# Performance work log

Hardware: AMD Instinct MI355X
Metric: run time of the kernel (lower is better)

## Reference

```python
import jax, jax.numpy as jnp
import numpy as np

N, C, T, H, W = 16, 64, 30, 64, 44
PC = 64
OUT_H, OUT_W = 16, 20
T_RATE, H_RATE, W_RATE = 0.4, 4.0 / 8, 10.0 / 11  # torso
HEAD_H_RATE = 1.0 / 8
EPS = 1e-8


def setup_inputs() -> dict:
    key = jax.random.key(0)
    ks = jax.random.split(key, 8)
    x = jax.random.normal(ks[0], (N, C, T, H, W), jnp.float32)
    param_x = jax.random.normal(ks[1], (N, PC), jnp.float32)
    W1 = jax.random.normal(ks[2], (PC, PC // 2), jnp.float32) * 0.1
    b1 = jnp.zeros((PC // 2,), jnp.float32)
    W2 = jax.random.normal(ks[3], (PC // 2, 7), jnp.float32) * 0.1
    b2 = jnp.zeros((7,), jnp.float32)
    Wf = jax.random.normal(ks[4], (C, C), jnp.float32) * 0.05
    bf = jnp.zeros((C,), jnp.float32)
    return {"x": x, "param_x": param_x, "W1": W1, "b1": b1, "W2": W2, "b2": b2, "Wf": Wf, "bf": bf}


def reference(x, param_x, W1, b1, W2, b2, Wf, bf):
    n, c, t, h, w = x.shape
    dtype = x.dtype
    atten_in_t = t * T_RATE
    atten_in_h = h * H_RATE
    atten_in_w = w * W_RATE
    atten_ratio = atten_in_w / atten_in_h
    aout_h = int(round(OUT_W / atten_ratio))
    anchor_t = int(round(t / 2.0))
    anchor_x = int(round(w / 2.0))
    anchor_y = int(round(atten_in_h / 2.0 + h * HEAD_H_RATE))  # torso anchor

    # --- localization MLP (locator stand-in): param_x -> 7 params per sample ---
    hid = jnp.tanh(param_x @ W1 + b1)
    p = hid @ W2 + b2  # [N, 7]
    dt0, dx0, dy0 = p[:, 0:1], p[:, 1:2], p[:, 2:3]
    log_sigma2, log_delta_t, log_delta, log_gamma = p[:, 3:4], p[:, 4:5], p[:, 5:6], p[:, 6:7]

    dx = jnp.tanh(dx0) * atten_in_w / 2.0 + anchor_x          # [N,1]
    dy = jnp.tanh(dy0) * atten_in_h / 2.0 + anchor_y          # [N,1]
    sigma2 = jnp.exp(log_sigma2)                              # [N,1]
    delta = jnp.exp(log_delta) * W_RATE                      # [N,1]
    gamma = jax.nn.sigmoid(log_gamma)                         # [N,1]

    # --- spatial Gaussian filter banks ---
    gx = jnp.arange(OUT_W, dtype=dtype)
    gy = jnp.arange(aout_h, dtype=dtype)
    mu_x = dx + (gx - OUT_W / 2.0) * delta                    # [N, OUT_W]
    mu_y = dy + (gy - aout_h / 2.0) * delta                   # [N, aout_h]
    a = jnp.arange(w, dtype=dtype)
    b = jnp.arange(h, dtype=dtype)
    s2 = sigma2[:, :, None]                                   # [N,1,1]
    Fx = jnp.exp(-((a - mu_x[:, :, None]) ** 2) / (2.0 * s2))  # [N, OUT_W, W]
    Fy = jnp.exp(-((b - mu_y[:, :, None]) ** 2) / (2.0 * s2))  # [N, aout_h, H]
    Fx = Fx / jnp.maximum(jnp.sum(Fx, -1, keepdims=True), EPS)
    Fy = Fy / jnp.maximum(jnp.sum(Fy, -1, keepdims=True), EPS)

    # --- spatial sampling: Fy @ x @ Fx^T over the (C*T)-folded batch dim ---
    x2 = x.reshape(n, c * t, h, w)
    t1 = jnp.einsum('ndhw,nqw->ndhq', x2, Fx)                 # [N, C*T, H, OUT_W]
    g = jnp.einsum('nph,ndhq->ndpq', Fy, t1)                  # [N, C*T, aout_h, OUT_W]
    pad_t = (OUT_H - aout_h) // 2
    pad_b = OUT_H - pad_t - aout_h
    g = jnp.pad(g, ((0, 0), (0, 0), (pad_t, pad_b), (0, 0)))  # [N, C*T, OUT_H, OUT_W]

    # --- temporal linear resampling (grid_sample, align_corners=True, zero pad) ---
    dt = jnp.tanh(dt0) * atten_in_t / 2.0 + anchor_t          # [N,1]
    delta_t = jnp.exp(log_delta_t) * T_RATE                   # [N,1]
    gt = jnp.arange(t, dtype=dtype)
    mu_t = dt + (gt - t / 2.0) * delta_t                      # [N, T] raw frame positions

    gseq = g.reshape(n, c, t, OUT_H * OUT_W).transpose(0, 1, 3, 2).reshape(n, c * OUT_H * OUT_W, t)
    i0f = jnp.floor(mu_t)
    frac = mu_t - i0f
    i0 = i0f.astype(jnp.int32)
    i1 = i0 + 1

    def gather(idx):
        return jnp.take_along_axis(gseq, jnp.clip(idx, 0, t - 1)[:, None, :], axis=2)

    w0 = jnp.where((i0 >= 0) & (i0 < t), 1.0 - frac, 0.0)[:, None, :]
    w1 = jnp.where((i1 >= 0) & (i1 < t), frac, 0.0)[:, None, :]
    samp = gather(i0) * w0 + gather(i1) * w1                  # [N, C*OUT_H*OUT_W, T]
    out = samp.reshape(n, c, OUT_H, OUT_W, t).transpose(0, 1, 4, 2, 3)  # [N,C,T,OUT_H,OUT_W]

    out = out * gamma.reshape(n, 1, 1, 1, 1)
    # feature extraction: pointwise Conv3d (extractor stand-in)
    out = jnp.einsum('ncthw,oc->nothw', out, Wf) + bf[None, :, None, None, None]

    params = jnp.stack([dt[:, 0], dx[:, 0], dy[:, 0], sigma2[:, 0],
                        delta[:, 0], delta_t[:, 0], gamma[:, 0]], 0)  # [7, N]
    return out, jax.lax.stop_gradient(params)
```

## Files before the change

kernel.cpp:

```cpp
#include <hip/hip_runtime.h>
#include <math.h>

#define NN 16
#define CC 64
#define TT 30
#define HH 64
#define WW 44
#define OUTH 16
#define OUTW 20
#define HW 320

#define FX_OFF    0
#define FY_OFF    14080
#define IDX0_OFF  30464
#define IDX1_OFF  30944
#define TW0_OFF   31424
#define TW1_OFF   31904
#define GAM_OFF   32384
#define G_OFF     32400

__global__ __launch_bounds__(64) void params_kernel(
    const float* __restrict__ param_x, const float* __restrict__ W1,
    const float* __restrict__ b1, const float* __restrict__ W2,
    const float* __restrict__ b2, float* __restrict__ ws,
    float* __restrict__ params_out) {
  int n = blockIdx.x;
  int tid = threadIdx.x;
  __shared__ float px[64];
  __shared__ float hid[32];
  __shared__ float pv[7];

  px[tid] = param_x[n * 64 + tid];
  __syncthreads();
  if (tid < 32) {
    float s = b1[tid];
    #pragma unroll
    for (int k = 0; k < 64; ++k) s += px[k] * W1[k * 32 + tid];
    hid[tid] = tanhf(s);
  }
  __syncthreads();
  if (tid < 7) {
    float s = b2[tid];
    #pragma unroll
    for (int j = 0; j < 32; ++j) s += hid[j] * W2[j * 7 + tid];
    pv[tid] = s;
  }
  __syncthreads();

  float dt      = tanhf(pv[0]) * 6.0f  + 15.0f;
  float dx      = tanhf(pv[1]) * 20.0f + 22.0f;
  float dy      = tanhf(pv[2]) * 16.0f + 24.0f;
  float sigma2  = expf(pv[3]);
  float delta_t = expf(pv[4]) * 0.4f;
  float delta   = expf(pv[5]) * (10.0f / 11.0f);
  float gamma   = 1.0f / (1.0f + expf(-pv[6]));
  float inv2s2  = 1.0f / (2.0f * sigma2);

  if (tid < 20) {
    float mu = dx + ((float)tid - 10.0f) * delta;
    float vals[44];
    float s = 0.0f;
    #pragma unroll
    for (int w = 0; w < 44; ++w) {
      float d = (float)w - mu;
      float e = expf(-d * d * inv2s2);
      vals[w] = e; s += e;
    }
    float inv = 1.0f / fmaxf(s, 1e-8f);
    float* Fx = ws + FX_OFF + n * (20 * 44) + tid * 44;
    #pragma unroll
    for (int w = 0; w < 44; ++w) Fx[w] = vals[w] * inv;
  }
  if (tid < 16) {
    float mu = dy + ((float)tid - 8.0f) * delta;
    float vals[64];
    float s = 0.0f;
    #pragma unroll
    for (int h = 0; h < 64; ++h) {
      float d = (float)h - mu;
      float e = expf(-d * d * inv2s2);
      vals[h] = e; s += e;
    }
    float inv = 1.0f / fmaxf(s, 1e-8f);
    float* Fy = ws + FY_OFF + n * (16 * 64) + tid * 64;
    #pragma unroll
    for (int h = 0; h < 64; ++h) Fy[h] = vals[h] * inv;
  }
  if (tid < 30) {
    float mu = dt + ((float)tid - 15.0f) * delta_t;
    float i0f = floorf(mu);
    float frac = mu - i0f;
    int i0 = (int)i0f;
    int i1 = i0 + 1;
    float w0 = (i0 >= 0 && i0 < TT) ? (1.0f - frac) : 0.0f;
    float w1 = (i1 >= 0 && i1 < TT) ? frac : 0.0f;
    ((int*)(ws + IDX0_OFF))[n * TT + tid] = min(max(i0, 0), TT - 1);
    ((int*)(ws + IDX1_OFF))[n * TT + tid] = min(max(i1, 0), TT - 1);
    ws[TW0_OFF + n * TT + tid] = w0;
    ws[TW1_OFF + n * TT + tid] = w1;
  }
  if (tid == 0) {
    ws[GAM_OFF + n] = gamma;
    params_out[0 * NN + n] = dt;
    params_out[1 * NN + n] = dx;
    params_out[2 * NN + n] = dy;
    params_out[3 * NN + n] = sigma2;
    params_out[4 * NN + n] = delta;
    params_out[5 * NN + n] = delta_t;
    params_out[6 * NN + n] = gamma;
  }
}

__global__ __launch_bounds__(256) void spatial_kernel(
    const float* __restrict__ x, const float* __restrict__ fxbuf,
    const float* __restrict__ fybuf, float* __restrict__ g) {
  int b = blockIdx.x;
  int n  = b / (TT * 16);
  int r  = b % (TT * 16);
  int t  = r / 16;
  int c0 = (r % 16) * 4;

  int tid  = threadIdx.x;
  int cl   = tid >> 6;
  int lane = tid & 63;

  __shared__ float st1[4 * 20 * 68];
  __shared__ float sFy[16 * 68];

  {
    const float* Fy = fybuf + n * (16 * 64);
    #pragma unroll
    for (int i = tid; i < 16 * 64; i += 256) {
      int p = i >> 6, h = i & 63;
      sFy[p * 68 + h] = Fy[i];
    }
  }

  int c = c0 + cl;
  const float* xs = x + ((((size_t)n * CC + c) * TT + t) * HH + lane) * WW;
  float xrow[44];
  {
    const float4* xp = (const float4*)xs;
    #pragma unroll
    for (int i = 0; i < 11; ++i) {
      float4 v = xp[i];
      xrow[4 * i + 0] = v.x; xrow[4 * i + 1] = v.y;
      xrow[4 * i + 2] = v.z; xrow[4 * i + 3] = v.w;
    }
  }
  const float* fx = fxbuf + n * (20 * 44);
  float acc[20];
  #pragma unroll
  for (int q = 0; q < 20; ++q) {
    float s = 0.0f;
    #pragma unroll
    for (int w = 0; w < 44; ++w) s = fmaf(xrow[w], fx[q * 44 + w], s);
    acc[q] = s;
  }
  #pragma unroll
  for (int q = 0; q < 20; ++q) st1[(cl * 20 + q) * 68 + lane] = acc[q];
  __syncthreads();

  int p  = lane >> 2;
  int qg = lane & 3;
  float o[5] = {0.f, 0.f, 0.f, 0.f, 0.f};
  #pragma unroll
  for (int hc = 0; hc < 16; ++hc) {
    float4 fy = *(const float4*)&sFy[p * 68 + hc * 4];
    #pragma unroll
    for (int j = 0; j < 5; ++j) {
      int q = qg * 5 + j;
      float4 tv = *(const float4*)&st1[(cl * 20 + q) * 68 + hc * 4];
      o[j] = fmaf(fy.x, tv.x, fmaf(fy.y, tv.y, fmaf(fy.z, tv.z, fmaf(fy.w, tv.w, o[j]))));
    }
  }
  float* gout = g + ((size_t)((n * CC + c) * TT + t)) * HW + p * OUTW + qg * 5;
  #pragma unroll
  for (int j = 0; j < 5; ++j) gout[j] = o[j];
}

__global__ __launch_bounds__(256) void output_kernel(
    const float* __restrict__ g, const float* __restrict__ ws,
    const float* __restrict__ Wf, const float* __restrict__ bf,
    float* __restrict__ out) {
  int b = blockIdx.x;
  int n    = b / (TT * 2);
  int r    = b % (TT * 2);
  int tp   = r >> 1;
  int hw0  = (r & 1) * 160;
  int tid  = threadIdx.x;

  __shared__ float sWfT[64 * 65];
  __shared__ float smix[64 * 160];

  #pragma unroll
  for (int i = tid; i < 64 * 64; i += 256) {
    int oc = i >> 6, c = i & 63;
    sWfT[c * 65 + oc] = Wf[i];
  }

  int i0 = ((const int*)(ws + IDX0_OFF))[n * TT + tp];
  int i1 = ((const int*)(ws + IDX1_OFF))[n * TT + tp];
  float w0 = ws[TW0_OFF + n * TT + tp];
  float w1 = ws[TW1_OFF + n * TT + tp];
  float gamma = ws[GAM_OFF + n];

  #pragma unroll
  for (int i = tid; i < 64 * 160; i += 256) {
    int c = i / 160, hwl = i % 160;
    size_t base = (size_t)(n * CC + c) * TT;
    float g0 = g[(base + i0) * HW + hw0 + hwl];
    float g1 = g[(base + i1) * HW + hw0 + hwl];
    smix[i] = gamma * (w0 * g0 + w1 * g1);
  }
  __syncthreads();

  int ocg = tid >> 5;
  int hwg = tid & 31;
  int oc0 = ocg * 8;
  int hwl0 = hwg * 5;
  float acc[8][5];
  #pragma unroll
  for (int u = 0; u < 8; ++u)
    #pragma unroll
    for (int j = 0; j < 5; ++j) acc[u][j] = 0.0f;

  #pragma unroll 4
  for (int c = 0; c < 64; ++c) {
    float4 wv0 = *(const float4*)&sWfT[c * 65 + oc0];
    float4 wv1 = *(const float4*)&sWfT[c * 65 + oc0 + 4];
    float m[5];
    #pragma unroll
    for (int j = 0; j < 5; ++j) m[j] = smix[c * 160 + hwl0 + j];
    float wv[8] = {wv0.x, wv0.y, wv0.z, wv0.w, wv1.x, wv1.y, wv1.z, wv1.w};
    #pragma unroll
    for (int u = 0; u < 8; ++u)
      #pragma unroll
      for (int j = 0; j < 5; ++j) acc[u][j] = fmaf(wv[u], m[j], acc[u][j]);
  }

  #pragma unroll
  for (int u = 0; u < 8; ++u) {
    int oc = oc0 + u;
    float bias = bf[oc];
    float* op = out + (((size_t)n * CC + oc) * TT + tp) * HW + hw0 + hwl0;
    #pragma unroll
    for (int j = 0; j < 5; ++j) op[j] = acc[u][j] + bias;
  }
}

extern "C" void kernel_launch(void* const* d_in, const int* in_sizes, int n_in,
                              void* d_out, int out_size, void* d_ws,
                              size_t ws_size, hipStream_t stream) {
  const float* x       = (const float*)d_in[0];
  const float* param_x = (const float*)d_in[1];
  const float* W1      = (const float*)d_in[2];
  const float* b1      = (const float*)d_in[3];
  const float* W2      = (const float*)d_in[4];
  const float* b2      = (const float*)d_in[5];
  const float* Wf      = (const float*)d_in[6];
  const float* bf      = (const float*)d_in[7];
  float* out = (float*)d_out;
  float* ws  = (float*)d_ws;
  float* params_out = out + (size_t)NN * CC * TT * HW;

  params_kernel<<<NN, 64, 0, stream>>>(param_x, W1, b1, W2, b2, ws, params_out);
  spatial_kernel<<<NN * TT * 16, 256, 0, stream>>>(
      x, ws + FX_OFF, ws + FY_OFF, ws + G_OFF);
  output_kernel<<<NN * TT * 2, 256, 0, stream>>>(ws + G_OFF, ws, Wf, bf, out);
}
```

Measured before the change: 549.6 us.

## Process 8 channels per spatial block and vectorize output kernel loads

```diff
diff --git a/kernel.cpp b/kernel.cpp
--- a/kernel.cpp
+++ b/kernel.cpp
@@ -115,68 +115,79 @@
     const float* __restrict__ x, const float* __restrict__ fxbuf,
     const float* __restrict__ fybuf, float* __restrict__ g) {
   int b = blockIdx.x;
-  int n  = b / (TT * 16);
-  int r  = b % (TT * 16);
-  int t  = r / 16;
-  int c0 = (r % 16) * 4;
-
-  int tid  = threadIdx.x;
-  int cl   = tid >> 6;
-  int lane = tid & 63;
-
-  __shared__ float st1[4 * 20 * 68];
+  int n  = b / (TT * 8);
+  int r  = b % (TT * 8);
+  int t  = r / 8;
+  int c0 = (r % 8) * 8;
+  int tid = threadIdx.x;
+
+  __shared__ float st1[8 * 20 * 68];
   __shared__ float sFy[16 * 68];
 
   {
     const float* Fy = fybuf + n * (16 * 64);
     #pragma unroll
     for (int i = tid; i < 16 * 64; i += 256) {
-      int p = i >> 6, h = i & 63;
-      sFy[p * 68 + h] = Fy[i];
-    }
-  }
-
-  int c = c0 + cl;
-  const float* xs = x + ((((size_t)n * CC + c) * TT + t) * HH + lane) * WW;
-  float xrow[44];
-  {
-    const float4* xp = (const float4*)xs;
+      sFy[(i >> 6) * 68 + (i & 63)] = Fy[i];
+    }
+  }
+
+  const float* fx = fxbuf + n * (20 * 44);
+  #pragma unroll
+  for (int k = 0; k < 2; ++k) {
+    int row = tid + k * 256;
+    int c = row >> 6;
+    int h = row & 63;
+    const float4* xp =
+        (const float4*)(x + ((((size_t)n * CC + c0 + c) * TT + t) * HH + h) * WW);
+    float xrow[44];
     #pragma unroll
     for (int i = 0; i < 11; ++i) {
       float4 v = xp[i];
       xrow[4 * i + 0] = v.x; xrow[4 * i + 1] = v.y;
       xrow[4 * i + 2] = v.z; xrow[4 * i + 3] = v.w;
     }
-  }
-  const float* fx = fxbuf + n * (20 * 44);
-  float acc[20];
-  #pragma unroll
-  for (int q = 0; q < 20; ++q) {
-    float s = 0.0f;
-    #pragma unroll
-    for (int w = 0; w < 44; ++w) s = fmaf(xrow[w], fx[q * 44 + w], s);
-    acc[q] = s;
-  }
-  #pragma unroll
-  for (int q = 0; q < 20; ++q) st1[(cl * 20 + q) * 68 + lane] = acc[q];
-  __syncthreads();
-
-  int p  = lane >> 2;
-  int qg = lane & 3;
-  float o[5] = {0.f, 0.f, 0.f, 0.f, 0.f};
+    #pragma unroll
+    for (int q = 0; q < 20; ++q) {
+      float s = 0.0f;
+      #pragma unroll
+      for (int w = 0; w < 44; ++w) s = fmaf(xrow[w], fx[q * 44 + w], s);
+      st1[(c * 20 + q) * 68 + h] = s;
+    }
+  }
+  __syncthreads();
+
+  int c  = tid >> 5;
+  int s5 = tid & 31;
+  int p0 = (s5 >> 2) * 2;
+  int q0 = (s5 & 3) * 5;
+  float acc[2][5];
+  #pragma unroll
+  for (int u = 0; u < 2; ++u)
+    #pragma unroll
+    for (int j = 0; j < 5; ++j) acc[u][j] = 0.0f;
+
   #pragma unroll
   for (int hc = 0; hc < 16; ++hc) {
-    float4 fy = *(const float4*)&sFy[p * 68 + hc * 4];
+    float4 fya = *(const float4*)&sFy[p0 * 68 + hc * 4];
+    float4 fyb = *(const float4*)&sFy[(p0 + 1) * 68 + hc * 4];
     #pragma unroll
     for (int j = 0; j < 5; ++j) {
-      int q = qg * 5 + j;
-      float4 tv = *(const float4*)&st1[(cl * 20 + q) * 68 + hc * 4];
-      o[j] = fmaf(fy.x, tv.x, fmaf(fy.y, tv.y, fmaf(fy.z, tv.z, fmaf(fy.w, tv.w, o[j]))));
-    }
-  }
-  float* gout = g + ((size_t)((n * CC + c) * TT + t)) * HW + p * OUTW + qg * 5;
-  #pragma unroll
-  for (int j = 0; j < 5; ++j) gout[j] = o[j];
+      float4 tv = *(const float4*)&st1[(c * 20 + q0 + j) * 68 + hc * 4];
+      acc[0][j] = fmaf(fya.x, tv.x, fmaf(fya.y, tv.y,
+                   fmaf(fya.z, tv.z, fmaf(fya.w, tv.w, acc[0][j]))));
+      acc[1][j] = fmaf(fyb.x, tv.x, fmaf(fyb.y, tv.y,
+                   fmaf(fyb.z, tv.z, fmaf(fyb.w, tv.w, acc[1][j]))));
+    }
+  }
+
+  float* gbase = g + ((size_t)((n * CC + c0 + c) * TT + t)) * HW;
+  #pragma unroll
+  for (int u = 0; u < 2; ++u) {
+    float* gp = gbase + (p0 + u) * OUTW + q0;
+    #pragma unroll
+    for (int j = 0; j < 5; ++j) gp[j] = acc[u][j];
+  }
 }
 
 __global__ __launch_bounds__(256) void output_kernel(
@@ -194,9 +205,13 @@
   __shared__ float smix[64 * 160];
 
   #pragma unroll
-  for (int i = tid; i < 64 * 64; i += 256) {
-    int oc = i >> 6, c = i & 63;
-    sWfT[c * 65 + oc] = Wf[i];
+  for (int i4 = tid; i4 < 64 * 16; i4 += 256) {
+    int oc = i4 >> 4, cb = (i4 & 15) * 4;
+    float4 v = *(const float4*)&Wf[oc * 64 + cb];
+    sWfT[(cb + 0) * 65 + oc] = v.x;
+    sWfT[(cb + 1) * 65 + oc] = v.y;
+    sWfT[(cb + 2) * 65 + oc] = v.z;
+    sWfT[(cb + 3) * 65 + oc] = v.w;
   }
 
   int i0 = ((const int*)(ws + IDX0_OFF))[n * TT + tp];
@@ -206,12 +221,17 @@
   float gamma = ws[GAM_OFF + n];
 
   #pragma unroll
-  for (int i = tid; i < 64 * 160; i += 256) {
-    int c = i / 160, hwl = i % 160;
+  for (int i4 = tid; i4 < 64 * 40; i4 += 256) {
+    int c = i4 / 40, off = (i4 % 40) * 4;
     size_t base = (size_t)(n * CC + c) * TT;
-    float g0 = g[(base + i0) * HW + hw0 + hwl];
-    float g1 = g[(base + i1) * HW + hw0 + hwl];
-    smix[i] = gamma * (w0 * g0 + w1 * g1);
+    float4 g0 = *(const float4*)&g[(base + i0) * HW + hw0 + off];
+    float4 g1 = *(const float4*)&g[(base + i1) * HW + hw0 + off];
+    float4 m;
+    m.x = gamma * (w0 * g0.x + w1 * g1.x);
+    m.y = gamma * (w0 * g0.y + w1 * g1.y);
+    m.z = gamma * (w0 * g0.z + w1 * g1.z);
+    m.w = gamma * (w0 * g0.w + w1 * g1.w);
+    *(float4*)&smix[c * 160 + off] = m;
   }
   __syncthreads();
 
@@ -265,7 +285,7 @@
   float* params_out = out + (size_t)NN * CC * TT * HW;
 
   params_kernel<<<NN, 64, 0, stream>>>(param_x, W1, b1, W2, b2, ws, params_out);
-  spatial_kernel<<<NN * TT * 16, 256, 0, stream>>>(
+  spatial_kernel<<<NN * TT * 8, 256, 0, stream>>>(
       x, ws + FX_OFF, ws + FY_OFF, ws + G_OFF);
   output_kernel<<<NN * TT * 2, 256, 0, stream>>>(ws + G_OFF, ws, Wf, bf, out);
 }
```

After: 555.0 us. Within noise of the previous version (+1.0%).
